# Kernel tuning notes

Measured on AMD Instinct MI355X. Metric: run time of the kernel, lower is better.

## Reference

```python
import jax, jax.numpy as jnp
import numpy as np

WINDOW_SIZE, SM, PS = 8, 2, 2  # window_size, spatial_merge_size, patch_size
SMU = SM * SM  # spatial_merge_unit


def _window_index(grid_thw):
    """Numpy port of get_window_index; returns permutation of arange(S)."""
    vmws = WINDOW_SIZE // SM // PS  # 2
    out, wid = [], 0
    for t, h, w in grid_thw:
        lh, lw = h // SM, w // SM
        idx = np.arange(t * lh * lw).reshape(t, lh, lw)
        ph = vmws - lh % vmws
        pw = vmws - lw % vmws
        nh, nw = (lh + ph) // vmws, (lw + pw) // vmws
        pad = np.full((t, lh + ph, lw + pw), -100, dtype=np.int64)
        pad[:, :lh, :lw] = idx
        pad = pad.reshape(t, nh, vmws, nw, vmws).transpose(0, 1, 3, 2, 4).reshape(-1)
        out.append(pad[pad != -100] + wid)
        wid += t * lh * lw
    return np.concatenate(out).astype(np.int32)


def setup_inputs() -> dict:
    key = jax.random.key(0)
    ks = jax.random.split(key, 5)
    B, T, C, H = 1, 16384, 1280, 16
    D = C // H  # 80
    grid_thw = np.array([[1, 256, 256]], dtype=np.int64)  # llm grid 128x128 -> S=16384
    wi = _window_index(grid_thw)
    x = jax.random.normal(ks[0], (B, T, C), jnp.float32)
    cos = jax.random.normal(ks[1], (B * T, 1, D), jnp.float32)
    sin = jax.random.normal(ks[2], (B * T, 1, D), jnp.float32)
    W_qkv = jax.random.normal(ks[3], (C, 3 * C), jnp.float32) * (C ** -0.5)
    W_proj = jax.random.normal(ks[4], (C, C), jnp.float32) * (C ** -0.5)
    # each window: (vmws*vmws) merged tokens * SMU patches = 16 tokens
    block_size = (WINDOW_SIZE // SM // PS) ** 2 * SMU
    return {"x": x, "cos": cos, "sin": sin, "W_qkv": W_qkv, "W_proj": W_proj,
            "window_index": jnp.asarray(wi), "block_size": block_size}


def reference(x, cos, sin, W_qkv, W_proj, window_index, block_size):
    B, T, C = x.shape
    S = B * T
    D = cos.shape[-1]
    H = C // D
    # window reorder (gather)
    xr = x.reshape(S, C)[window_index]
    qkv = (xr @ W_qkv).reshape(S, 3, H, D)
    q, k, v = qkv[:, 0], qkv[:, 1], qkv[:, 2]
    # module's (unusual) q/k mixing 'rotary'
    cw, sw = cos[window_index], sin[window_index]  # (S,1,D) broadcast over heads
    qr = q * cw + k * sw
    kr = k * cw - q * sw
    # block-diagonal attention: uniform 16-token windows -> reshape, no SxS mask
    nb = S // block_size
    qb = qr.reshape(nb, block_size, H, D)
    kb = kr.reshape(nb, block_size, H, D)
    vb = v.reshape(nb, block_size, H, D)
    att = jnp.einsum('bqhd,bkhd->bhqk', qb, kb) * (D ** -0.5)
    att = jax.nn.softmax(att, axis=-1)
    y = jnp.einsum('bhqk,bkhd->bqhd', att, vb).reshape(S, C)
    # undo window reorder
    y = y[jnp.argsort(window_index)]
    return y.reshape(B, T, C) @ W_proj
```

## Files before the change

### kernel.cpp

```cpp
#include <hip/hip_runtime.h>
#include <hip/hip_bf16.h>

#define S_TOK   16384
#define C_DIM   1280
#define C3_DIM  3840
#define H_DIM   16
#define D_DIM   80
#define BLK     16

using u16x8  = __attribute__((ext_vector_type(8))) unsigned short;
using u16x4  = __attribute__((ext_vector_type(4))) unsigned short;
using bf16x8 = __attribute__((ext_vector_type(8))) __bf16;
using f32x4  = __attribute__((ext_vector_type(4))) float;

__device__ __forceinline__ unsigned short f2bf(float f) {
    return __bfloat16_as_ushort(__float2bfloat16(f));
}
__device__ __forceinline__ float bf2f(unsigned short u) {
    unsigned int x = (unsigned int)u << 16;
    return __builtin_bit_cast(float, x);
}
__device__ __forceinline__ void gload_lds16(const unsigned short* g, unsigned short* l) {
    __builtin_amdgcn_global_load_lds(
        (const __attribute__((address_space(1))) void*)g,
        (__attribute__((address_space(3))) void*)l, 16, 0, 0);
}

__global__ __launch_bounds__(256) void transpose_cvt(
    const float* __restrict__ W, unsigned short* __restrict__ WT, int K, int N)
{
    __shared__ float tile[32][33];
    const int n0 = blockIdx.x * 32, k0 = blockIdx.y * 32;
    const int tx = threadIdx.x & 31, ty = threadIdx.x >> 5;
#pragma unroll
    for (int i = ty; i < 32; i += 8)
        tile[i][tx] = W[(size_t)(k0 + i) * N + n0 + tx];
    __syncthreads();
#pragma unroll
    for (int i = ty; i < 32; i += 8)
        WT[(size_t)(n0 + i) * K + k0 + tx] = f2bf(tile[tx][i]);
}

__global__ __launch_bounds__(256) void gather_cvt(
    const float* __restrict__ x, const int* __restrict__ wi,
    unsigned short* __restrict__ xg)
{
    int idx = blockIdx.x * 256 + threadIdx.x;
    int s  = idx / 160;
    int c8 = (idx - s * 160) * 8;
    const float* src = x + (size_t)wi[s] * C_DIM + c8;
    f32x4 v0 = *(const f32x4*)src;
    f32x4 v1 = *(const f32x4*)(src + 4);
    u16x8 o;
    o[0]=f2bf(v0[0]); o[1]=f2bf(v0[1]); o[2]=f2bf(v0[2]); o[3]=f2bf(v0[3]);
    o[4]=f2bf(v1[0]); o[5]=f2bf(v1[1]); o[6]=f2bf(v1[2]); o[7]=f2bf(v1[3]);
    *(u16x8*)&xg[(size_t)s * C_DIM + c8] = o;
}

#define TM 128
#define TN 128
#define BK 64

template<bool OUTF32>
__global__ __launch_bounds__(256) void gemm_mfma(
    const unsigned short* __restrict__ A,
    const unsigned short* __restrict__ BT,
    void* __restrict__ Cp,
    int N, int K)
{
    __shared__ __align__(16) unsigned short As[TM * BK];
    __shared__ __align__(16) unsigned short Bs[TN * BK];

    const int m0   = blockIdx.x * TM;
    const int n0   = blockIdx.y * TN;
    const int tid  = threadIdx.x;
    const int lane = tid & 63;
    const int wv   = tid >> 6;
    const int wm   = (wv >> 1) * 64;
    const int wn   = (wv & 1) * 64;
    const int lrow = lane & 15;
    const int quad = lane >> 4;

    int r_[4], csw[4];
#pragma unroll
    for (int c = 0; c < 4; c++) {
        int ch = (wv * 4 + c) * 64 + lane;
        r_[c]  = ch >> 3;
        csw[c] = ((ch & 7) ^ (r_[c] & 7)) << 3;
    }

    int aoff[4], asw[4], boff[4], bsw[4];
#pragma unroll
    for (int t = 0; t < 4; t++) {
        int ra = wm + t * 16 + lrow;
        aoff[t] = ra << 7;  asw[t] = (ra & 7) << 4;
        int rb = wn + t * 16 + lrow;
        boff[t] = rb << 7;  bsw[t] = (rb & 7) << 4;
    }

    f32x4 acc[4][4];
#pragma unroll
    for (int i = 0; i < 4; i++)
#pragma unroll
        for (int j = 0; j < 4; j++)
            acc[i][j] = (f32x4){0.f, 0.f, 0.f, 0.f};

    for (int kt = 0; kt < K; kt += BK) {
#pragma unroll
        for (int c = 0; c < 4; c++)
            gload_lds16(A + (size_t)(m0 + r_[c]) * K + kt + csw[c],
                        As + (wv * 4 + c) * 512);
#pragma unroll
        for (int c = 0; c < 4; c++)
            gload_lds16(BT + (size_t)(n0 + r_[c]) * K + kt + csw[c],
                        Bs + (wv * 4 + c) * 512);
        __syncthreads();

#pragma unroll
        for (int ks = 0; ks < BK; ks += 32) {
            const int cb = (ks << 1) + (quad << 4);
            bf16x8 af[4], bfr[4];
#pragma unroll
            for (int mt = 0; mt < 4; mt++)
                af[mt] = *(const bf16x8*)((const char*)As +
                                          aoff[mt] + (cb ^ asw[mt]));
#pragma unroll
            for (int nt = 0; nt < 4; nt++)
                bfr[nt] = *(const bf16x8*)((const char*)Bs +
                                           boff[nt] + (cb ^ bsw[nt]));
#pragma unroll
            for (int mt = 0; mt < 4; mt++)
#pragma unroll
                for (int nt = 0; nt < 4; nt++)
                    acc[mt][nt] = __builtin_amdgcn_mfma_f32_16x16x32_bf16(
                        af[mt], bfr[nt], acc[mt][nt], 0, 0, 0);
        }
        __syncthreads();
    }

#pragma unroll
    for (int mt = 0; mt < 4; mt++)
#pragma unroll
        for (int nt = 0; nt < 4; nt++)
#pragma unroll
            for (int r = 0; r < 4; r++) {
                int row = m0 + wm + mt * 16 + quad * 4 + r;
                int col = n0 + wn + nt * 16 + lrow;
                if (OUTF32)
                    ((float*)Cp)[(size_t)row * N + col] = acc[mt][nt][r];
                else
                    ((unsigned short*)Cp)[(size_t)row * N + col] =
                        f2bf(acc[mt][nt][r]);
            }
}

__global__ __launch_bounds__(256) void attn_fused(
    const unsigned short* __restrict__ qkv,
    const float* __restrict__ cosp,
    const float* __restrict__ sinp,
    const int* __restrict__ wi,
    unsigned short* __restrict__ y)
{
    const int wave = threadIdx.x >> 6;
    const int lane = threadIdx.x & 63;
    const int b    = blockIdx.y;
    const int h    = blockIdx.x * 4 + wave;
    const int j16  = lane & 15;
    const int quad = lane >> 4;

    const int    srow = b * BLK + j16;
    const int    crow = wi[srow];
    const size_t qoff = (size_t)srow * C3_DIM + h * D_DIM;

    const unsigned short* vbase =
        qkv + (size_t)b * BLK * C3_DIM + 2 * C_DIM + h * D_DIM + j16;
    u16x8 vraw[5];
#pragma unroll
    for (int t = 0; t < 5; t++) {
#pragma unroll
        for (int e = 0; e < 8; e++) {
            int kks = (quad < 2) ? (quad * 8 + e) : e;
            unsigned short rv = vbase[(size_t)kks * C3_DIM + t * 16];
            vraw[t][e] = (quad < 2) ? rv : (unsigned short)0;
        }
    }

    const unsigned short* qrow = qkv + qoff;
    const float* cr = cosp + (size_t)crow * D_DIM;
    const float* sr = sinp + (size_t)crow * D_DIM;
    bf16x8 qf[3], kf[3];
#pragma unroll
    for (int s = 0; s < 3; s++) {
        int d = 32 * s + quad * 8;
        bool valid = (d < D_DIM);
        int dc = valid ? d : 0;
        u16x8 qv = *(const u16x8*)(qrow + dc);
        u16x8 kv = *(const u16x8*)(qrow + C_DIM + dc);
        f32x4 c0 = *(const f32x4*)(cr + dc);
        f32x4 c1 = *(const f32x4*)(cr + dc + 4);
        f32x4 s0 = *(const f32x4*)(sr + dc);
        f32x4 s1 = *(const f32x4*)(sr + dc + 4);
        u16x8 qo, ko;
#pragma unroll
        for (int j = 0; j < 8; j++) {
            float cw = (j < 4) ? c0[j] : c1[j - 4];
            float sw = (j < 4) ? s0[j] : s1[j - 4];
            float q = bf2f(qv[j]), k = bf2f(kv[j]);
            qo[j] = valid ? f2bf(q * cw + k * sw) : (unsigned short)0;
            ko[j] = valid ? f2bf(k * cw - q * sw) : (unsigned short)0;
        }
        qf[s] = __builtin_bit_cast(bf16x8, qo);
        kf[s] = __builtin_bit_cast(bf16x8, ko);
    }

    f32x4 sacc = (f32x4){0.f, 0.f, 0.f, 0.f};
#pragma unroll
    for (int s = 0; s < 3; s++)
        sacc = __builtin_amdgcn_mfma_f32_16x16x32_bf16(kf[s], qf[s], sacc, 0, 0, 0);

    const float scale = 0.11180339887498948f;
    float sc[4];
#pragma unroll
    for (int r = 0; r < 4; r++) sc[r] = sacc[r] * scale;
    float m = fmaxf(fmaxf(sc[0], sc[1]), fmaxf(sc[2], sc[3]));
    m = fmaxf(m, __shfl_xor(m, 16));
    m = fmaxf(m, __shfl_xor(m, 32));
    float e[4], sum = 0.f;
#pragma unroll
    for (int r = 0; r < 4; r++) { e[r] = __expf(sc[r] - m); sum += e[r]; }
    sum += __shfl_xor(sum, 16);
    sum += __shfl_xor(sum, 32);
    float inv = 1.f / sum;

    int sl = quad * 32 + j16;
    float pv0[4], pv1[4];
#pragma unroll
    for (int r = 0; r < 4; r++) pv0[r] = __shfl(e[r], sl & 63);
#pragma unroll
    for (int r = 0; r < 4; r++) pv1[r] = __shfl(e[r], (sl + 16) & 63);
    u16x8 pf;
#pragma unroll
    for (int r = 0; r < 4; r++) {
        pf[r]     = (quad < 2) ? f2bf(pv0[r]) : (unsigned short)0;
        pf[r + 4] = (quad < 2) ? f2bf(pv1[r]) : (unsigned short)0;
    }
    bf16x8 pfrag = __builtin_bit_cast(bf16x8, pf);

    unsigned short* yrow = y + (size_t)crow * C_DIM + h * D_DIM + quad * 4;
#pragma unroll
    for (int t = 0; t < 5; t++) {
        f32x4 o = __builtin_amdgcn_mfma_f32_16x16x32_bf16(
            __builtin_bit_cast(bf16x8, vraw[t]), pfrag,
            (f32x4){0.f, 0.f, 0.f, 0.f}, 0, 0, 0);
        u16x4 ov;
#pragma unroll
        for (int r = 0; r < 4; r++) ov[r] = f2bf(o[r] * inv);
        *(u16x4*)(yrow + t * 16) = ov;
    }
}

extern "C" void kernel_launch(void* const* d_in, const int* in_sizes, int n_in,
                              void* d_out, int out_size, void* d_ws, size_t ws_size,
                              hipStream_t stream)
{
    const float* x     = (const float*)d_in[0];
    const float* cosp  = (const float*)d_in[1];
    const float* sinp  = (const float*)d_in[2];
    const float* Wqkv  = (const float*)d_in[3];
    const float* Wproj = (const float*)d_in[4];
    const int*   wi    = (const int*)d_in[5];

    char* ws = (char*)d_ws;
    unsigned short* qkv    = (unsigned short*)ws;
    unsigned short* yun    = (unsigned short*)(ws + 125829120ull);
    unsigned short* wqkvT  = (unsigned short*)(ws + 167772160ull);
    unsigned short* wprojT = (unsigned short*)(ws + 177602560ull);
    unsigned short* xg     = (unsigned short*)(ws + 180879360ull);

    transpose_cvt<<<dim3(C3_DIM / 32, C_DIM / 32), 256, 0, stream>>>(
        Wqkv, wqkvT, C_DIM, C3_DIM);
    transpose_cvt<<<dim3(C_DIM / 32, C_DIM / 32), 256, 0, stream>>>(
        Wproj, wprojT, C_DIM, C_DIM);

    gather_cvt<<<S_TOK * 160 / 256, 256, 0, stream>>>(x, wi, xg);

    gemm_mfma<false><<<dim3(S_TOK / TM, C3_DIM / TN), 256, 0, stream>>>(
        xg, wqkvT, qkv, C3_DIM, C_DIM);

    attn_fused<<<dim3(H_DIM / 4, S_TOK / BLK), 256, 0, stream>>>(
        qkv, cosp, sinp, wi, yun);

    gemm_mfma<true><<<dim3(S_TOK / TM, C_DIM / TN), 256, 0, stream>>>(
        yun, wprojT, d_out, C_DIM, C_DIM);
}
```

Measured before the change: 501.0 us.

## Store QKV GEMM output as head-major Q/K/V planes for attention

The QKV GEMM epilogue now writes its output into three separate planes (Q, K, V), each laid out per head as [h][token][d], instead of a row-major [token][3C] matrix. The attention kernel reads Q, K and V from these planes, so one head's 16-token window is a contiguous 16x80 chunk rather than rows spaced 3840 elements apart. The aim is better locality and coalescing for the attention loads. In exchange, the GEMM stores become strided by 80 elements per row, which may scatter the epilogue writes.

```diff
diff --git a/kernel.cpp b/kernel.cpp
--- a/kernel.cpp
+++ b/kernel.cpp
@@ -7,6 +7,7 @@
 #define H_DIM   16
 #define D_DIM   80
 #define BLK     16
+#define PLANE_ELEMS ((size_t)S_TOK * C_DIM)
 
 using u16x8  = __attribute__((ext_vector_type(8))) unsigned short;
 using u16x4  = __attribute__((ext_vector_type(4))) unsigned short;
@@ -61,7 +62,7 @@
 #define TN 128
 #define BK 64
 
-template<bool OUTF32>
+template<int OUTMODE>
 __global__ __launch_bounds__(256) void gemm_mfma(
     const unsigned short* __restrict__ A,
     const unsigned short* __restrict__ BT,
@@ -139,23 +140,35 @@
     }
 
 #pragma unroll
-    for (int mt = 0; mt < 4; mt++)
-#pragma unroll
-        for (int nt = 0; nt < 4; nt++)
+    for (int nt = 0; nt < 4; nt++) {
+        const int cb = n0 + wn + nt * 16;
+        unsigned short* pb = nullptr;
+        if (OUTMODE == 2) {
+            int which = cb / C_DIM;
+            int hc    = cb - which * C_DIM;
+            int h     = hc / D_DIM;
+            int d0    = hc - h * D_DIM;
+            pb = (unsigned short*)Cp + (size_t)which * PLANE_ELEMS
+               + (size_t)h * S_TOK * D_DIM + d0 + lrow;
+        }
+#pragma unroll
+        for (int mt = 0; mt < 4; mt++)
 #pragma unroll
             for (int r = 0; r < 4; r++) {
                 int row = m0 + wm + mt * 16 + quad * 4 + r;
-                int col = n0 + wn + nt * 16 + lrow;
-                if (OUTF32)
-                    ((float*)Cp)[(size_t)row * N + col] = acc[mt][nt][r];
+                if (OUTMODE == 0)
+                    ((float*)Cp)[(size_t)row * N + cb + lrow] = acc[mt][nt][r];
+                else if (OUTMODE == 1)
+                    ((unsigned short*)Cp)[(size_t)row * N + cb + lrow] =
+                        f2bf(acc[mt][nt][r]);
                 else
-                    ((unsigned short*)Cp)[(size_t)row * N + col] =
-                        f2bf(acc[mt][nt][r]);
+                    pb[(size_t)row * D_DIM] = f2bf(acc[mt][nt][r]);
             }
+    }
 }
 
 __global__ __launch_bounds__(256) void attn_fused(
-    const unsigned short* __restrict__ qkv,
+    const unsigned short* __restrict__ planes,
     const float* __restrict__ cosp,
     const float* __restrict__ sinp,
     const int* __restrict__ wi,
@@ -168,24 +181,24 @@
     const int j16  = lane & 15;
     const int quad = lane >> 4;
 
-    const int    srow = b * BLK + j16;
-    const int    crow = wi[srow];
-    const size_t qoff = (size_t)srow * C3_DIM + h * D_DIM;
-
-    const unsigned short* vbase =
-        qkv + (size_t)b * BLK * C3_DIM + 2 * C_DIM + h * D_DIM + j16;
+    const int srow = b * BLK + j16;
+    const int crow = wi[srow];
+
+    const unsigned short* Vb = planes + 2 * PLANE_ELEMS
+        + ((size_t)h * S_TOK + b * BLK) * D_DIM + j16;
     u16x8 vraw[5];
 #pragma unroll
     for (int t = 0; t < 5; t++) {
 #pragma unroll
         for (int e = 0; e < 8; e++) {
             int kks = (quad < 2) ? (quad * 8 + e) : e;
-            unsigned short rv = vbase[(size_t)kks * C3_DIM + t * 16];
+            unsigned short rv = Vb[(size_t)kks * D_DIM + t * 16];
             vraw[t][e] = (quad < 2) ? rv : (unsigned short)0;
         }
     }
 
-    const unsigned short* qrow = qkv + qoff;
+    const unsigned short* Qr = planes + ((size_t)h * S_TOK + srow) * D_DIM;
+    const unsigned short* Kr = Qr + PLANE_ELEMS;
     const float* cr = cosp + (size_t)crow * D_DIM;
     const float* sr = sinp + (size_t)crow * D_DIM;
     bf16x8 qf[3], kf[3];
@@ -194,8 +207,8 @@
         int d = 32 * s + quad * 8;
         bool valid = (d < D_DIM);
         int dc = valid ? d : 0;
-        u16x8 qv = *(const u16x8*)(qrow + dc);
-        u16x8 kv = *(const u16x8*)(qrow + C_DIM + dc);
+        u16x8 qv = *(const u16x8*)(Qr + dc);
+        u16x8 kv = *(const u16x8*)(Kr + dc);
         f32x4 c0 = *(const f32x4*)(cr + dc);
         f32x4 c1 = *(const f32x4*)(cr + dc + 4);
         f32x4 s0 = *(const f32x4*)(sr + dc);
@@ -271,7 +284,7 @@
     const int*   wi    = (const int*)d_in[5];
 
     char* ws = (char*)d_ws;
-    unsigned short* qkv    = (unsigned short*)ws;
+    unsigned short* planes = (unsigned short*)ws;
     unsigned short* yun    = (unsigned short*)(ws + 125829120ull);
     unsigned short* wqkvT  = (unsigned short*)(ws + 167772160ull);
     unsigned short* wprojT = (unsigned short*)(ws + 177602560ull);
@@ -284,12 +297,12 @@
 
     gather_cvt<<<S_TOK * 160 / 256, 256, 0, stream>>>(x, wi, xg);
 
-    gemm_mfma<false><<<dim3(S_TOK / TM, C3_DIM / TN), 256, 0, stream>>>(
-        xg, wqkvT, qkv, C3_DIM, C_DIM);
+    gemm_mfma<2><<<dim3(S_TOK / TM, C3_DIM / TN), 256, 0, stream>>>(
+        xg, wqkvT, planes, C3_DIM, C_DIM);
 
     attn_fused<<<dim3(H_DIM / 4, S_TOK / BLK), 256, 0, stream>>>(
-        qkv, cosp, sinp, wi, yun);
-
-    gemm_mfma<true><<<dim3(S_TOK / TM, C_DIM / TN), 256, 0, stream>>>(
+        planes, cosp, sinp, wi, yun);
+
+    gemm_mfma<0><<<dim3(S_TOK / TM, C_DIM / TN), 256, 0, stream>>>(
         yun, wprojT, d_out, C_DIM, C_DIM);
 }
```

Measured after the change: 476.8 us. 4.8% less time.
